# Optimization experiments

Hardware: AMD Instinct MI355X
Metric: run time of the kernel (lower is better)

Reference implementation:

```python
import jax, jax.numpy as jnp
import numpy as np

T, B, E = 2048, 16, 1024   # time, batch, embed_dim (fairseq T x B x C layout)
CDIM = 1024                # conv_dim
H = 16                     # num_heads
K = 31                     # kernel_size, padding_l = K-1 (causal left pad)


def _xavier(k, shape):
    fan_out, fan_in = shape
    lim = float(np.sqrt(6.0 / (fan_in + fan_out)))
    return jax.random.uniform(k, shape, jnp.float32, -lim, lim)


def setup_inputs() -> dict:
    key = jax.random.key(0)
    ks = jax.random.split(key, 5)
    return {
        "x": jax.random.normal(ks[0], (T, B, E), jnp.float32),
        "w1": _xavier(ks[1], (CDIM, E)),
        "b1": jnp.zeros((CDIM,), jnp.float32),
        "ww": _xavier(ks[2], (H * K, CDIM)),  # DynamicConv weight_linear
        "bw": jnp.zeros((H * K,), jnp.float32),
        "w2": _xavier(ks[3], (E, CDIM)),
        "b2": jnp.zeros((E,), jnp.float32),
        "gamma": jnp.ones((E,), jnp.float32),
        "beta": jnp.zeros((E,), jnp.float32),
    }


def layer_norm(x, g, b, eps=1e-5):
    m = x.mean(-1, keepdims=True)
    v = ((x - m) ** 2).mean(-1, keepdims=True)
    return (x - m) * jax.lax.rsqrt(v + eps) * g + b


def dynamic_conv(h, ww, bw):
    # h: [T, B, C]; per-position softmax kernel weights shared across R=C/H channels per head
    Tn, Bn, C = h.shape
    R = C // H
    w = jax.nn.softmax((h @ ww.T + bw).reshape(Tn, Bn, H, K), axis=-1)  # [T,B,H,K]
    hp = jnp.pad(h.reshape(Tn, Bn, H, R), ((K - 1, 0), (0, 0), (0, 0), (0, 0)))
    # out[t] = sum_k w[t,:,:,k] * h[t + k - (K-1)]  (causal banded aggregation)
    acc = jnp.zeros((Tn, Bn, H, R), h.dtype)
    for k in range(K):  # fixed small kernel-size loop, not a data-dim loop
        acc = acc + w[:, :, :, k:k + 1] * hp[k:k + Tn]
    return acc.reshape(Tn, Bn, C)


def reference(x, w1, b1, ww, bw, w2, b2, gamma, beta):
    # eval mode: all dropouts are identity; normalize_before=False -> LN after residual
    h = x @ w1.T + b1            # linear1: [T,B,E] -> [T,B,CDIM]
    h = dynamic_conv(h, ww, bw)  # DynamicConv, weight_softmax=True, no conv bias
    h = h @ w2.T + b2            # linear2: back to embed_dim
    return layer_norm(x + h, gamma, beta)
```

## Files before the change

### kernel.cpp

```cpp
#include <hip/hip_runtime.h>

#define T_DIM 2048
#define B_DIM 16
#define E_DIM 1024
#define CD    1024
#define NH    16
#define KSZ   31
#define M_DIM 32768
#define SLICE 131072
#define BSTRIDE 2097152

typedef unsigned int u32;
typedef unsigned short u16;
typedef __attribute__((ext_vector_type(8))) __bf16 bf16x8;
typedef __attribute__((ext_vector_type(4))) float f32x4;
typedef __attribute__((ext_vector_type(4))) float fvec4;
typedef __attribute__((ext_vector_type(8))) unsigned short us8;
typedef __attribute__((ext_vector_type(4))) unsigned short us4;
typedef __attribute__((ext_vector_type(4))) unsigned int ui4;

__device__ __forceinline__ float bf2f(u16 u) {
  union { float f; u32 i; } c; c.i = ((u32)u) << 16; return c.f;
}
__device__ __forceinline__ u16 f2bf(float f) {
  union { float f; u32 i; } c; c.f = f;
  u32 u = c.i;
  u += 0x7fffu + ((u >> 16) & 1u);
  return (u16)(u >> 16);
}

#define GLDS(gp, lp)                                                        \
  __builtin_amdgcn_global_load_lds(                                         \
      (__attribute__((address_space(1))) void*)(gp),                        \
      (__attribute__((address_space(3))) void*)(lp), 16, 0, 0)

__global__ __launch_bounds__(256) void prep(const float* __restrict__ x,
                                            const float* __restrict__ w1,
                                            const float* __restrict__ w2,
                                            const float* __restrict__ ww,
                                            u16* __restrict__ xbt,
                                            u16* __restrict__ w1b,
                                            u16* __restrict__ w2b,
                                            u16* __restrict__ wwb,
                                            u16* __restrict__ zreg)
{
  const int NX = (T_DIM * B_DIM * E_DIM) / 4;
  const int N1 = NX + (CD * E_DIM) / 4;
  const int N2 = N1 + (E_DIM * CD) / 4;
  const int N3 = N2 + (NH * KSZ * CD) / 4;
  int i = blockIdx.x * 256 + threadIdx.x;
  if (i < NX) {
    int rr = i >> 8, c = i & 255;
    int t = rr >> 4, b = rr & 15;
    fvec4 v = ((const fvec4*)x)[i];
    us4 o;
    o[0] = f2bf(v[0]); o[1] = f2bf(v[1]); o[2] = f2bf(v[2]); o[3] = f2bf(v[3]);
    ((us4*)xbt)[(size_t)(b * T_DIM + t) * 256 + c] = o;
  } else if (i < N1) {
    int j = i - NX;
    fvec4 v = ((const fvec4*)w1)[j];
    us4 o;
    o[0] = f2bf(v[0]); o[1] = f2bf(v[1]); o[2] = f2bf(v[2]); o[3] = f2bf(v[3]);
    ((us4*)w1b)[j] = o;
  } else if (i < N2) {
    int j = i - N1;
    fvec4 v = ((const fvec4*)w2)[j];
    us4 o;
    o[0] = f2bf(v[0]); o[1] = f2bf(v[1]); o[2] = f2bf(v[2]); o[3] = f2bf(v[3]);
    ((us4*)w2b)[j] = o;
  } else if (i < N3) {
    int j = i - N2;
    fvec4 v = ((const fvec4*)ww)[j];
    us4 o;
    o[0] = f2bf(v[0]); o[1] = f2bf(v[1]); o[2] = f2bf(v[2]); o[3] = f2bf(v[3]);
    ((us4*)wwb)[j] = o;
  } else {
    ((ui4*)zreg)[i - N3] = (ui4)(0u);
  }
}

template<int OUT_MODE, int GUARD_N, int A_CONV>
__global__ __launch_bounds__(512, 2) void gemm256(
    const u16* __restrict__ A, const u16* __restrict__ B,
    const float* __restrict__ bias, void* __restrict__ Cout,
    int N, int K, int ldc, int ntn)
{
  __shared__ u16 sA[2][256 * 64];
  __shared__ u16 sB[2][256 * 64];
  const int tid = threadIdx.x;
  const int lane = tid & 63;
  const int wid = tid >> 6;
  const int wr = wid >> 2;
  const int wc = wid & 3;

  const int swz = (blockIdx.x & 7) * (gridDim.x >> 3) + (blockIdx.x >> 3);
  const int bm = (swz / ntn) * 256;
  const int bn = (swz % ntn) * 256;

  const int srow = tid >> 3;
  const int scol = (tid & 7) * 8;
  const int scols = scol ^ ((srow & 7) << 3);
  const int sdst = srow * 64 + scol;

  const u16* gA[4];
  #pragma unroll
  for (int st = 0; st < 4; st++) {
    int rr = bm + st * 64 + srow;
    if (A_CONV)
      gA[st] = A + (size_t)(rr >> 11) * BSTRIDE + (size_t)(rr & 2047) * 64 + scols;
    else
      gA[st] = A + (size_t)rr * K + scols;
  }
  const u16* gB[4];
  #pragma unroll
  for (int st = 0; st < 4; st++) {
    int br = bn + st * 64 + srow;
    if (GUARD_N) br = min(br, N - 1);
    gB[st] = B + (size_t)br * K + scols;
  }

  f32x4 acc[8][4];
  #pragma unroll
  for (int i = 0; i < 8; i++)
    #pragma unroll
    for (int j = 0; j < 4; j++) acc[i][j] = (f32x4)(0.0f);

  const int fr = lane & 15;
  const int g8 = (lane >> 4) * 8;
  const int sx = (fr & 7) << 3;

  const int NT = K >> 6;
  int buf = 0;

  #pragma unroll
  for (int st = 0; st < 4; st++) GLDS(gB[st], &sB[0][st * 4096 + sdst]);
  #pragma unroll
  for (int st = 0; st < 4; st++) GLDS(gA[st], &sA[0][st * 4096 + sdst]);
  asm volatile("s_waitcnt vmcnt(0)" ::: "memory");
  __builtin_amdgcn_s_barrier();

  for (int kt = 0; kt < NT; kt++) {
    const bool more = (kt + 1 < NT);
    const size_t koA = A_CONV ? (size_t)(kt + 1) * SLICE : (size_t)(kt + 1) * 64;
    const size_t koB = (size_t)(kt + 1) * 64;
    u16* dA = &sA[buf ^ 1][0];
    u16* dB = &sB[buf ^ 1][0];

    bf16x8 bF[4][2];
    #pragma unroll
    for (int n = 0; n < 4; n++)
      #pragma unroll
      for (int kh = 0; kh < 2; kh++) {
        int row = wc * 64 + n * 16 + fr;
        bF[n][kh] = *(const bf16x8*)&sB[buf][row * 64 + ((kh * 32 + g8) ^ sx)];
      }
    bf16x8 aF[2][2];
    #pragma unroll
    for (int mi = 0; mi < 2; mi++)
      #pragma unroll
      for (int kh = 0; kh < 2; kh++) {
        int row = wr * 128 + mi * 16 + fr;
        aF[mi][kh] = *(const bf16x8*)&sA[buf][row * 64 + ((kh * 32 + g8) ^ sx)];
      }
    if (more) {
      GLDS(gB[0] + koB, dB + 0 * 4096 + sdst);
      GLDS(gB[1] + koB, dB + 1 * 4096 + sdst);
    }
    __builtin_amdgcn_s_barrier();
    asm volatile("s_waitcnt lgkmcnt(0)" ::: "memory");
    __builtin_amdgcn_sched_barrier(0);
    __builtin_amdgcn_s_setprio(1);
    #pragma unroll
    for (int mi = 0; mi < 2; mi++)
      #pragma unroll
      for (int n = 0; n < 4; n++)
        #pragma unroll
        for (int kh = 0; kh < 2; kh++)
          acc[mi][n] = __builtin_amdgcn_mfma_f32_16x16x32_bf16(aF[mi][kh], bF[n][kh], acc[mi][n], 0, 0, 0);
    __builtin_amdgcn_s_setprio(0);
    __builtin_amdgcn_sched_barrier(0);
    __builtin_amdgcn_s_barrier();

    {
      bf16x8 aG[2][2];
      #pragma unroll
      for (int mi = 0; mi < 2; mi++)
        #pragma unroll
        for (int kh = 0; kh < 2; kh++) {
          int row = wr * 128 + (2 + mi) * 16 + fr;
          aG[mi][kh] = *(const bf16x8*)&sA[buf][row * 64 + ((kh * 32 + g8) ^ sx)];
        }
      if (more) {
        GLDS(gB[2] + koB, dB + 2 * 4096 + sdst);
        GLDS(gB[3] + koB, dB + 3 * 4096 + sdst);
      }
      __builtin_amdgcn_s_barrier();
      asm volatile("s_waitcnt lgkmcnt(0)" ::: "memory");
      __builtin_amdgcn_sched_barrier(0);
      __builtin_amdgcn_s_setprio(1);
      #pragma unroll
      for (int mi = 0; mi < 2; mi++)
        #pragma unroll
        for (int n = 0; n < 4; n++)
          #pragma unroll
          for (int kh = 0; kh < 2; kh++)
            acc[2 + mi][n] = __builtin_amdgcn_mfma_f32_16x16x32_bf16(aG[mi][kh], bF[n][kh], acc[2 + mi][n], 0, 0, 0);
      __builtin_amdgcn_s_setprio(0);
      __builtin_amdgcn_sched_barrier(0);
      if (more) { asm volatile("s_waitcnt vmcnt(4)" ::: "memory"); }
      else      { asm volatile("s_waitcnt vmcnt(0)" ::: "memory"); }
      __builtin_amdgcn_s_barrier();
    }

    {
      bf16x8 aG[2][2];
      #pragma unroll
      for (int mi = 0; mi < 2; mi++)
        #pragma unroll
        for (int kh = 0; kh < 2; kh++) {
          int row = wr * 128 + (4 + mi) * 16 + fr;
          aG[mi][kh] = *(const bf16x8*)&sA[buf][row * 64 + ((kh * 32 + g8) ^ sx)];
        }
      if (more) {
        GLDS(gA[0] + koA, dA + 0 * 4096 + sdst);
        GLDS(gA[2] + koA, dA + 2 * 4096 + sdst);
      }
      __builtin_amdgcn_s_barrier();
      asm volatile("s_waitcnt lgkmcnt(0)" ::: "memory");
      __builtin_amdgcn_sched_barrier(0);
      __builtin_amdgcn_s_setprio(1);
      #pragma unroll
      for (int mi = 0; mi < 2; mi++)
        #pragma unroll
        for (int n = 0; n < 4; n++)
          #pragma unroll
          for (int kh = 0; kh < 2; kh++)
            acc[4 + mi][n] = __builtin_amdgcn_mfma_f32_16x16x32_bf16(aG[mi][kh], bF[n][kh], acc[4 + mi][n], 0, 0, 0);
      __builtin_amdgcn_s_setprio(0);
      __builtin_amdgcn_sched_barrier(0);
      __builtin_amdgcn_s_barrier();
    }

    {
      bf16x8 aG[2][2];
      #pragma unroll
      for (int mi = 0; mi < 2; mi++)
        #pragma unroll
        for (int kh = 0; kh < 2; kh++) {
          int row = wr * 128 + (6 + mi) * 16 + fr;
          aG[mi][kh] = *(const bf16x8*)&sA[buf][row * 64 + ((kh * 32 + g8) ^ sx)];
        }
      if (more) {
        GLDS(gA[1] + koA, dA + 1 * 4096 + sdst);
        GLDS(gA[3] + koA, dA + 3 * 4096 + sdst);
      }
      __builtin_amdgcn_s_barrier();
      asm volatile("s_waitcnt lgkmcnt(0)" ::: "memory");
      __builtin_amdgcn_sched_barrier(0);
      __builtin_amdgcn_s_setprio(1);
      #pragma unroll
      for (int mi = 0; mi < 2; mi++)
        #pragma unroll
        for (int n = 0; n < 4; n++)
          #pragma unroll
          for (int kh = 0; kh < 2; kh++)
            acc[6 + mi][n] = __builtin_amdgcn_mfma_f32_16x16x32_bf16(aG[mi][kh], bF[n][kh], acc[6 + mi][n], 0, 0, 0);
      __builtin_amdgcn_s_setprio(0);
      __builtin_amdgcn_sched_barrier(0);
      if (more) {
        asm volatile("s_waitcnt vmcnt(2)" ::: "memory");
      }
      __builtin_amdgcn_s_barrier();
    }
    buf ^= 1;
  }

  const int orow0 = bm + wr * 128 + (lane >> 4) * 4;
  const int ocol0 = bn + wc * 64 + fr;
  #pragma unroll
  for (int m = 0; m < 8; m++) {
    #pragma unroll
    for (int n = 0; n < 4; n++) {
      #pragma unroll
      for (int q = 0; q < 4; q++) {
        int row = orow0 + m * 16 + q;
        int col = ocol0 + n * 16;
        if (!GUARD_N || col < N) {
          float v = acc[m][n][q] + bias[col];
          if (OUT_MODE == 1) {
            ((u16*)Cout)[(size_t)row * ldc + col] = f2bf(v);
          } else if (OUT_MODE == 2) {
            int bb = row >> 11, t = row & 2047;
            int hh = col / 31, kk = col - hh * 31;
            ((u16*)Cout)[((size_t)((bb * NH + hh) * T_DIM + t)) * 32 + kk] = f2bf(v);
          } else {
            int bb = row >> 11, t = row & 2047;
            ((u16*)Cout)[(size_t)((bb << 4) + (col >> 6)) * SLICE + (size_t)t * 64 + (col & 63)] = f2bf(v);
          }
        }
      }
    }
  }
}

__global__ __launch_bounds__(256) void dconv(const u16* __restrict__ h1,
                                             const u16* __restrict__ wt,
                                             const u16* __restrict__ zreg,
                                             u16* __restrict__ outc)
{
  constexpr int TT = 128, HALO = 30, SW = 33;
  int bid = blockIdx.x;
  int tt = bid & 15;
  int b  = (bid >> 4) & 15;
  int h  = bid >> 8;
  int s  = b * 16 + h;
  int t0 = tt * TT;
  __shared__ u16 hl[(TT + HALO) * 64];
  __shared__ float wl[TT * SW];
  int tid = threadIdx.x;

  const u16* slice = h1 + (size_t)s * SLICE;
  #pragma unroll
  for (int it = 0; it < 5; it++) {
    int c = it * 256 + tid;
    if (c < (TT + HALO) * 8) {
      int row = t0 - HALO + (c >> 3);
      const u16* src = slice + (size_t)row * 64 + (c & 7) * 8;
      if (row < 0) src = zreg + (c & 7) * 8;
      GLDS(src, hl + c * 8);
    }
  }
  {
    const u16* wsrc = wt + ((size_t)s * T_DIM + t0) * 32;
    #pragma unroll
    for (int it = 0; it < 2; it++) {
      int j = (it * 256 + tid) * 8;
      us8 v = *(const us8*)(wsrc + j);
      int row = j >> 5, col = j & 31;
      #pragma unroll
      for (int e = 0; e < 8; e++) wl[row * SW + col + e] = bf2f(v[e]);
    }
  }
  __syncthreads();

  if (tid < TT) {
    float* p = wl + tid * SW;
    float v[KSZ];
    float mx = -1e30f;
    #pragma unroll
    for (int k = 0; k < KSZ; k++) { v[k] = p[k]; mx = fmaxf(mx, v[k]); }
    float sum = 0.f;
    #pragma unroll
    for (int k = 0; k < KSZ; k++) { v[k] = __expf(v[k] - mx); sum += v[k]; }
    float inv = 1.0f / sum;
    #pragma unroll
    for (int k = 0; k < KSZ; k++) p[k] = v[k] * inv;
  }
  __syncthreads();

  int rb = (tid & 7) * 8;
  int tl = tid >> 3;

  #pragma unroll
  for (int half = 0; half < 4; half++) {
    const int tb = tl + half * 32;
    const float* wp = wl + tb * SW;
    const u16* hb = hl + tb * 64 + rb;
    float acc[8];
    #pragma unroll
    for (int e = 0; e < 8; e++) acc[e] = 0.f;
    #pragma unroll
    for (int k = 0; k < KSZ; k++) {
      us8 hv = *(const us8*)(hb + k * 64);
      float w = wp[k];
      #pragma unroll
      for (int e = 0; e < 8; e++) acc[e] += w * bf2f(hv[e]);
    }
    us8 o;
    #pragma unroll
    for (int e = 0; e < 8; e++) o[e] = f2bf(acc[e]);
    *(us8*)(outc + (size_t)s * SLICE + (size_t)(t0 + tb) * 64 + rb) = o;
  }
}

__global__ __launch_bounds__(256) void ln_res(const u16* __restrict__ xb,
                                              const u16* __restrict__ hb,
                                              float* __restrict__ out,
                                              const float* __restrict__ gamma,
                                              const float* __restrict__ beta)
{
  int mp = blockIdx.x;
  int b = mp >> 11, t = mp & 2047;
  int xrow = t * 16 + b;
  const us4* xr = (const us4*)(xb + (size_t)mp * E_DIM);
  const us4* hr = (const us4*)(hb + (size_t)mp * E_DIM);
  fvec4* yr = (fvec4*)(out + (size_t)xrow * E_DIM);
  int tid = threadIdx.x;
  us4 hv = hr[tid];
  us4 xv = xr[tid];
  fvec4 s;
  #pragma unroll
  for (int e = 0; e < 4; e++) s[e] = bf2f(xv[e]) + bf2f(hv[e]);
  float sum = s[0] + s[1] + s[2] + s[3];
  float sq  = s[0]*s[0] + s[1]*s[1] + s[2]*s[2] + s[3]*s[3];
  #pragma unroll
  for (int off = 32; off >= 1; off >>= 1) {
    sum += __shfl_xor(sum, off, 64);
    sq  += __shfl_xor(sq, off, 64);
  }
  __shared__ float red[8];
  int lane = tid & 63, wid = tid >> 6;
  if (lane == 0) { red[wid] = sum; red[4 + wid] = sq; }
  __syncthreads();
  sum = red[0] + red[1] + red[2] + red[3];
  sq  = red[4] + red[5] + red[6] + red[7];
  float mean = sum * (1.0f / E_DIM);
  float var  = sq * (1.0f / E_DIM) - mean * mean;
  float rstd = rsqrtf(var + 1e-5f);
  fvec4 g = ((const fvec4*)gamma)[tid];
  fvec4 be = ((const fvec4*)beta)[tid];
  fvec4 o;
  #pragma unroll
  for (int e = 0; e < 4; e++) o[e] = (s[e] - mean) * rstd * g[e] + be[e];
  yr[tid] = o;
}

extern "C" void kernel_launch(void* const* d_in, const int* in_sizes, int n_in,
                              void* d_out, int out_size, void* d_ws, size_t ws_size,
                              hipStream_t stream)
{
  const float* x     = (const float*)d_in[0];
  const float* w1    = (const float*)d_in[1];
  const float* b1    = (const float*)d_in[2];
  const float* ww    = (const float*)d_in[3];
  const float* bw    = (const float*)d_in[4];
  const float* w2    = (const float*)d_in[5];
  const float* b2    = (const float*)d_in[6];
  const float* gamma = (const float*)d_in[7];
  const float* beta  = (const float*)d_in[8];
  float* out = (float*)d_out;

  char* ws = (char*)d_ws;
  u16*   xbt  = (u16*)(ws);
  u16*   h1p  = (u16*)(ws + ((size_t)64 << 20));
  u16*   wt   = (u16*)(ws + ((size_t)128 << 20));
  u16*   convp = (u16*)(ws + ((size_t)160 << 20));
  u16*   w1b  = (u16*)(ws + ((size_t)224 << 20));
  u16*   w2b  = (u16*)(ws + ((size_t)226 << 20));
  u16*   wwb  = (u16*)(ws + ((size_t)228 << 20));
  u16*   zreg = (u16*)(ws + ((size_t)230 << 20));
  u16*   h2p  = h1p;

  prep<<<35313, 256, 0, stream>>>(x, w1, w2, ww, xbt, w1b, w2b, wwb, zreg);

  gemm256<3, 0, 0><<<512, 512, 0, stream>>>(xbt, w1b, b1, h1p, CD, E_DIM, 0, 4);
  gemm256<2, 1, 1><<<256, 512, 0, stream>>>(h1p, wwb, bw, wt, NH * KSZ, CD, 0, 2);
  dconv<<<4096, 256, 0, stream>>>(h1p, wt, zreg, convp);
  gemm256<1, 0, 1><<<512, 512, 0, stream>>>(convp, w2b, b2, h2p, E_DIM, CD, E_DIM, 4);
  ln_res<<<32768, 256, 0, stream>>>(xbt, h2p, out, gamma, beta);
}
```

Before: 347.7 us.

## Restructure GEMM LDS pipeline into four half-K slots with deeper prefetch

Splits each 64-wide K tile into two 32-wide halves held in a 4-slot LDS ring instead of a 2-buffer 64-wide layout, with a new XOR swizzle suited to 32-element rows. Global-to-LDS loads are issued one and a half tiles ahead, which keeps more loads in flight and lowers fragment register pressure per phase. The aim is better overlap of memory and MFMA work. In exchange the waitcnt bookkeeping is more intricate, and a miscounted vmcnt could let compute read data that has not finished loading.

```diff
diff --git a/kernel.cpp b/kernel.cpp
--- a/kernel.cpp
+++ b/kernel.cpp
@@ -85,8 +85,8 @@
     const float* __restrict__ bias, void* __restrict__ Cout,
     int N, int K, int ldc, int ntn)
 {
-  __shared__ u16 sA[2][256 * 64];
-  __shared__ u16 sB[2][256 * 64];
+  __shared__ u16 sA[4][256 * 32];
+  __shared__ u16 sB[4][256 * 32];
   const int tid = threadIdx.x;
   const int lane = tid & 63;
   const int wid = tid >> 6;
@@ -97,27 +97,34 @@
   const int bm = (swz / ntn) * 256;
   const int bn = (swz % ntn) * 256;
 
-  const int srow = tid >> 3;
-  const int scol = (tid & 7) * 8;
-  const int scols = scol ^ ((srow & 7) << 3);
-  const int sdst = srow * 64 + scol;
-
-  const u16* gA[4];
-  #pragma unroll
-  for (int st = 0; st < 4; st++) {
-    int rr = bm + st * 64 + srow;
+  const int srow2 = tid >> 2;
+  const int scol2 = (tid & 3) * 8;
+  const int scol2s = scol2 ^ (((srow2 >> 1) & 3) << 3);
+  const int sdst2 = srow2 * 32 + scol2;
+
+  const u16* gA2[2];
+  const u16* gB2[2];
+  #pragma unroll
+  for (int st = 0; st < 2; st++) {
+    int rr = bm + st * 128 + srow2;
     if (A_CONV)
-      gA[st] = A + (size_t)(rr >> 11) * BSTRIDE + (size_t)(rr & 2047) * 64 + scols;
+      gA2[st] = A + (size_t)(rr >> 11) * BSTRIDE + (size_t)(rr & 2047) * 64 + scol2s;
     else
-      gA[st] = A + (size_t)rr * K + scols;
-  }
-  const u16* gB[4];
-  #pragma unroll
-  for (int st = 0; st < 4; st++) {
-    int br = bn + st * 64 + srow;
+      gA2[st] = A + (size_t)rr * K + scol2s;
+    int br = bn + st * 128 + srow2;
     if (GUARD_N) br = min(br, N - 1);
-    gB[st] = B + (size_t)br * K + scols;
-  }
+    gB2[st] = B + (size_t)br * K + scol2s;
+  }
+
+  auto stage = [&](int kt, int kh) {
+    int slot = (2 * kt + kh) & 3;
+    size_t koA = A_CONV ? (size_t)kt * SLICE + kh * 32 : (size_t)kt * 64 + kh * 32;
+    size_t koB = (size_t)kt * 64 + kh * 32;
+    GLDS(gA2[0] + koA, &sA[slot][0 * 4096 + sdst2]);
+    GLDS(gA2[1] + koA, &sA[slot][1 * 4096 + sdst2]);
+    GLDS(gB2[0] + koB, &sB[slot][0 * 4096 + sdst2]);
+    GLDS(gB2[1] + koB, &sB[slot][1 * 4096 + sdst2]);
+  };
 
   f32x4 acc[8][4];
   #pragma unroll
@@ -127,152 +134,87 @@
 
   const int fr = lane & 15;
   const int g8 = (lane >> 4) * 8;
-  const int sx = (fr & 7) << 3;
+
+  auto ard = [&](const u16* base, int row) -> bf16x8 {
+    return *(const bf16x8*)&base[row * 32 + (g8 ^ ((((row >> 1) & 3)) << 3))];
+  };
 
   const int NT = K >> 6;
-  int buf = 0;
-
-  #pragma unroll
-  for (int st = 0; st < 4; st++) GLDS(gB[st], &sB[0][st * 4096 + sdst]);
-  #pragma unroll
-  for (int st = 0; st < 4; st++) GLDS(gA[st], &sA[0][st * 4096 + sdst]);
-  asm volatile("s_waitcnt vmcnt(0)" ::: "memory");
+
+  stage(0, 0); stage(0, 1); stage(1, 0);
+  asm volatile("s_waitcnt vmcnt(8)" ::: "memory");
   __builtin_amdgcn_s_barrier();
 
   for (int kt = 0; kt < NT; kt++) {
-    const bool more = (kt + 1 < NT);
-    const size_t koA = A_CONV ? (size_t)(kt + 1) * SLICE : (size_t)(kt + 1) * 64;
-    const size_t koB = (size_t)(kt + 1) * 64;
-    u16* dA = &sA[buf ^ 1][0];
-    u16* dB = &sB[buf ^ 1][0];
-
-    bf16x8 bF[4][2];
-    #pragma unroll
-    for (int n = 0; n < 4; n++)
-      #pragma unroll
-      for (int kh = 0; kh < 2; kh++) {
-        int row = wc * 64 + n * 16 + fr;
-        bF[n][kh] = *(const bf16x8*)&sB[buf][row * 64 + ((kh * 32 + g8) ^ sx)];
-      }
-    bf16x8 aF[2][2];
-    #pragma unroll
-    for (int mi = 0; mi < 2; mi++)
-      #pragma unroll
-      for (int kh = 0; kh < 2; kh++) {
-        int row = wr * 128 + mi * 16 + fr;
-        aF[mi][kh] = *(const bf16x8*)&sA[buf][row * 64 + ((kh * 32 + g8) ^ sx)];
-      }
-    if (more) {
-      GLDS(gB[0] + koB, dB + 0 * 4096 + sdst);
-      GLDS(gB[1] + koB, dB + 1 * 4096 + sdst);
-    }
+    const int s0 = (2 * kt) & 3;
+    const int s1 = (2 * kt + 1) & 3;
+
+    bf16x8 bF[4], aG[4];
+    #pragma unroll
+    for (int n = 0; n < 4; n++) bF[n] = ard(&sB[s0][0], wc * 64 + n * 16 + fr);
+    #pragma unroll
+    for (int mi = 0; mi < 4; mi++) aG[mi] = ard(&sA[s0][0], wr * 128 + mi * 16 + fr);
+    if (kt + 1 < NT) stage(kt + 1, 1);
+    asm volatile("s_waitcnt lgkmcnt(0)" ::: "memory");
     __builtin_amdgcn_s_barrier();
+    __builtin_amdgcn_sched_barrier(0);
+    __builtin_amdgcn_s_setprio(1);
+    #pragma unroll
+    for (int mi = 0; mi < 4; mi++)
+      #pragma unroll
+      for (int n = 0; n < 4; n++)
+        acc[mi][n] = __builtin_amdgcn_mfma_f32_16x16x32_bf16(aG[mi], bF[n], acc[mi][n], 0, 0, 0);
+    __builtin_amdgcn_s_setprio(0);
+    __builtin_amdgcn_sched_barrier(0);
+
+    #pragma unroll
+    for (int mi = 0; mi < 4; mi++) aG[mi] = ard(&sA[s0][0], wr * 128 + (4 + mi) * 16 + fr);
     asm volatile("s_waitcnt lgkmcnt(0)" ::: "memory");
+    if (kt < NT - 1) { asm volatile("s_waitcnt vmcnt(8)" ::: "memory"); }
+    else             { asm volatile("s_waitcnt vmcnt(0)" ::: "memory"); }
+    __builtin_amdgcn_s_barrier();
     __builtin_amdgcn_sched_barrier(0);
     __builtin_amdgcn_s_setprio(1);
     #pragma unroll
-    for (int mi = 0; mi < 2; mi++)
+    for (int mi = 0; mi < 4; mi++)
       #pragma unroll
       for (int n = 0; n < 4; n++)
-        #pragma unroll
-        for (int kh = 0; kh < 2; kh++)
-          acc[mi][n] = __builtin_amdgcn_mfma_f32_16x16x32_bf16(aF[mi][kh], bF[n][kh], acc[mi][n], 0, 0, 0);
+        acc[4 + mi][n] = __builtin_amdgcn_mfma_f32_16x16x32_bf16(aG[mi], bF[n], acc[4 + mi][n], 0, 0, 0);
     __builtin_amdgcn_s_setprio(0);
     __builtin_amdgcn_sched_barrier(0);
+
+    #pragma unroll
+    for (int n = 0; n < 4; n++) bF[n] = ard(&sB[s1][0], wc * 64 + n * 16 + fr);
+    #pragma unroll
+    for (int mi = 0; mi < 4; mi++) aG[mi] = ard(&sA[s1][0], wr * 128 + mi * 16 + fr);
+    if (kt + 2 < NT) stage(kt + 2, 0);
+    asm volatile("s_waitcnt lgkmcnt(0)" ::: "memory");
     __builtin_amdgcn_s_barrier();
-
-    {
-      bf16x8 aG[2][2];
-      #pragma unroll
-      for (int mi = 0; mi < 2; mi++)
-        #pragma unroll
-        for (int kh = 0; kh < 2; kh++) {
-          int row = wr * 128 + (2 + mi) * 16 + fr;
-          aG[mi][kh] = *(const bf16x8*)&sA[buf][row * 64 + ((kh * 32 + g8) ^ sx)];
-        }
-      if (more) {
-        GLDS(gB[2] + koB, dB + 2 * 4096 + sdst);
-        GLDS(gB[3] + koB, dB + 3 * 4096 + sdst);
-      }
-      __builtin_amdgcn_s_barrier();
-      asm volatile("s_waitcnt lgkmcnt(0)" ::: "memory");
-      __builtin_amdgcn_sched_barrier(0);
-      __builtin_amdgcn_s_setprio(1);
-      #pragma unroll
-      for (int mi = 0; mi < 2; mi++)
-        #pragma unroll
-        for (int n = 0; n < 4; n++)
-          #pragma unroll
-          for (int kh = 0; kh < 2; kh++)
-            acc[2 + mi][n] = __builtin_amdgcn_mfma_f32_16x16x32_bf16(aG[mi][kh], bF[n][kh], acc[2 + mi][n], 0, 0, 0);
-      __builtin_amdgcn_s_setprio(0);
-      __builtin_amdgcn_sched_barrier(0);
-      if (more) { asm volatile("s_waitcnt vmcnt(4)" ::: "memory"); }
-      else      { asm volatile("s_waitcnt vmcnt(0)" ::: "memory"); }
-      __builtin_amdgcn_s_barrier();
-    }
-
-    {
-      bf16x8 aG[2][2];
-      #pragma unroll
-      for (int mi = 0; mi < 2; mi++)
-        #pragma unroll
-        for (int kh = 0; kh < 2; kh++) {
-          int row = wr * 128 + (4 + mi) * 16 + fr;
-          aG[mi][kh] = *(const bf16x8*)&sA[buf][row * 64 + ((kh * 32 + g8) ^ sx)];
-        }
-      if (more) {
-        GLDS(gA[0] + koA, dA + 0 * 4096 + sdst);
-        GLDS(gA[2] + koA, dA + 2 * 4096 + sdst);
-      }
-      __builtin_amdgcn_s_barrier();
-      asm volatile("s_waitcnt lgkmcnt(0)" ::: "memory");
-      __builtin_amdgcn_sched_barrier(0);
-      __builtin_amdgcn_s_setprio(1);
-      #pragma unroll
-      for (int mi = 0; mi < 2; mi++)
-        #pragma unroll
-        for (int n = 0; n < 4; n++)
-          #pragma unroll
-          for (int kh = 0; kh < 2; kh++)
-            acc[4 + mi][n] = __builtin_amdgcn_mfma_f32_16x16x32_bf16(aG[mi][kh], bF[n][kh], acc[4 + mi][n], 0, 0, 0);
-      __builtin_amdgcn_s_setprio(0);
-      __builtin_amdgcn_sched_barrier(0);
-      __builtin_amdgcn_s_barrier();
-    }
-
-    {
-      bf16x8 aG[2][2];
-      #pragma unroll
-      for (int mi = 0; mi < 2; mi++)
-        #pragma unroll
-        for (int kh = 0; kh < 2; kh++) {
-          int row = wr * 128 + (6 + mi) * 16 + fr;
-          aG[mi][kh] = *(const bf16x8*)&sA[buf][row * 64 + ((kh * 32 + g8) ^ sx)];
-        }
-      if (more) {
-        GLDS(gA[1] + koA, dA + 1 * 4096 + sdst);
-        GLDS(gA[3] + koA, dA + 3 * 4096 + sdst);
-      }
-      __builtin_amdgcn_s_barrier();
-      asm volatile("s_waitcnt lgkmcnt(0)" ::: "memory");
-      __builtin_amdgcn_sched_barrier(0);
-      __builtin_amdgcn_s_setprio(1);
-      #pragma unroll
-      for (int mi = 0; mi < 2; mi++)
-        #pragma unroll
-        for (int n = 0; n < 4; n++)
-          #pragma unroll
-          for (int kh = 0; kh < 2; kh++)
-            acc[6 + mi][n] = __builtin_amdgcn_mfma_f32_16x16x32_bf16(aG[mi][kh], bF[n][kh], acc[6 + mi][n], 0, 0, 0);
-      __builtin_amdgcn_s_setprio(0);
-      __builtin_amdgcn_sched_barrier(0);
-      if (more) {
-        asm volatile("s_waitcnt vmcnt(2)" ::: "memory");
-      }
-      __builtin_amdgcn_s_barrier();
-    }
-    buf ^= 1;
+    __builtin_amdgcn_sched_barrier(0);
+    __builtin_amdgcn_s_setprio(1);
+    #pragma unroll
+    for (int mi = 0; mi < 4; mi++)
+      #pragma unroll
+      for (int n = 0; n < 4; n++)
+        acc[mi][n] = __builtin_amdgcn_mfma_f32_16x16x32_bf16(aG[mi], bF[n], acc[mi][n], 0, 0, 0);
+    __builtin_amdgcn_s_setprio(0);
+    __builtin_amdgcn_sched_barrier(0);
+
+    #pragma unroll
+    for (int mi = 0; mi < 4; mi++) aG[mi] = ard(&sA[s1][0], wr * 128 + (4 + mi) * 16 + fr);
+    asm volatile("s_waitcnt lgkmcnt(0)" ::: "memory");
+    if (kt < NT - 2)      { asm volatile("s_waitcnt vmcnt(8)" ::: "memory"); }
+    else if (kt == NT - 2){ asm volatile("s_waitcnt vmcnt(4)" ::: "memory"); }
+    __builtin_amdgcn_s_barrier();
+    __builtin_amdgcn_sched_barrier(0);
+    __builtin_amdgcn_s_setprio(1);
+    #pragma unroll
+    for (int mi = 0; mi < 4; mi++)
+      #pragma unroll
+      for (int n = 0; n < 4; n++)
+        acc[4 + mi][n] = __builtin_amdgcn_mfma_f32_16x16x32_bf16(aG[mi], bF[n], acc[4 + mi][n], 0, 0, 0);
+    __builtin_amdgcn_s_setprio(0);
+    __builtin_amdgcn_sched_barrier(0);
   }
 
   const int orow0 = bm + wr * 128 + (lane >> 4) * 4;
```

Measured after the change: 350.0 us. Within noise of the previous version (+0.7%).
